# Kernel tuning notes

Hardware: AMD Instinct MI355X
Metric: run time of the kernel (lower is better)

Reference implementation:

```python
import jax, jax.numpy as jnp
import numpy as np

B, S, D, H, HD = 2, 2048, 1024, 16, 64


def setup_inputs() -> dict:
    key = jax.random.key(0)
    ks = jax.random.split(key, 11)
    scale_in = 1.0 / np.sqrt(D)
    return {
        "query": jax.random.normal(ks[0], (B, S, D), jnp.float32),
        "key": jax.random.normal(ks[1], (B, S, D), jnp.float32),
        "value": jax.random.normal(ks[2], (B, S, D), jnp.float32),
        "Wq": jax.random.normal(ks[3], (H, D, HD), jnp.float32) * scale_in,
        "bq": jax.random.normal(ks[4], (H, HD), jnp.float32) * 0.02,
        "Wk": jax.random.normal(ks[5], (H, D, HD), jnp.float32) * scale_in,
        "bk": jax.random.normal(ks[6], (H, HD), jnp.float32) * 0.02,
        "Wv": jax.random.normal(ks[7], (H, D, HD), jnp.float32) * scale_in,
        "bv": jax.random.normal(ks[8], (H, HD), jnp.float32) * 0.02,
        "Wo": jax.random.normal(ks[9], (D, D), jnp.float32) * scale_in,
        "bo": jax.random.normal(ks[10], (D,), jnp.float32) * 0.02,
    }


def reference(query, key, value, Wq, bq, Wk, bk, Wv, bv, Wo, bo):
    # Per-head projections, batched over heads (equivalent to the ModuleList loop).
    q = jnp.einsum('bsd,hdk->bhsk', query, Wq) + bq[None, :, None, :]   # [B,H,S,HD]
    k = jnp.einsum('bsd,hdk->bhsk', key, Wk) + bk[None, :, None, :]
    v = jnp.einsum('bsd,hdk->bhsk', value, Wv) + bv[None, :, None, :]
    scale = 1.0 / jnp.sqrt(jnp.asarray(q.shape[-1], q.dtype))
    scores = jnp.einsum('bhsk,bhtk->bhst', q, k) * scale                # [B,H,S,S]
    attn = jax.nn.softmax(scores, axis=-1)
    ctx = jnp.einsum('bhst,bhtk->bhsk', attn, v)                        # [B,H,S,HD]
    # Concat heads along last dim: [B,S,H*HD] == [B,S,D]
    x = jnp.transpose(ctx, (0, 2, 1, 3)).reshape(ctx.shape[0], ctx.shape[2], -1)
    return x @ Wo + bo
```

## Files before the change

kernel.cpp:

```cpp
#include <hip/hip_runtime.h>
#include <hip/hip_bf16.h>

typedef __bf16 bf16;
typedef __bf16 bf16x8 __attribute__((ext_vector_type(8)));
typedef __bf16 bf16x4 __attribute__((ext_vector_type(4)));
typedef __bf16 bf16x2 __attribute__((ext_vector_type(2)));
typedef float floatx4 __attribute__((ext_vector_type(4)));
typedef float floatx16 __attribute__((ext_vector_type(16)));

#define B_SZ 2
#define S_LEN 2048
#define D_DIM 1024
#define H_CNT 16
#define HD_DIM 64
#define M_ROWS 4096
#define QSCALE 0.18033688011112042f

__device__ __forceinline__ void async_ld16(const bf16* g, bf16* s) {
    __builtin_amdgcn_global_load_lds((const __attribute__((address_space(1))) void*)g,
                                     (__attribute__((address_space(3))) void*)s, 16, 0, 0);
}

__device__ __forceinline__ floatx4 mfma16(bf16x8 a, bf16x8 b, floatx4 c) {
    return __builtin_amdgcn_mfma_f32_16x16x32_bf16(a, b, c, 0, 0, 0);
}
__device__ __forceinline__ floatx16 mfma32(bf16x8 a, bf16x8 b, floatx16 c) {
    return __builtin_amdgcn_mfma_f32_32x32x16_bf16(a, b, c, 0, 0, 0);
}

struct PrepArgs {
    const float* cast_src[3]; bf16* cast_dst[3];
    const float* w_src[3];    bf16* w_dst[3];
    const float* wo;          bf16* wo_t;
};
__global__ __launch_bounds__(256) void prep(PrepArgs a) {
    __shared__ bf16 tile[32][33];
    const int bx = blockIdx.x, tid = threadIdx.x;
    if (bx < 12288) {
        const int t = bx >> 12, blk = bx & 4095;
        const float* s = a.cast_src[t];
        bf16* d = a.cast_dst[t];
        size_t i = ((size_t)blk * 256 + tid) * 4;
        float4 v = *(const float4*)(s + i);
        bf16x4 o = { (bf16)v.x, (bf16)v.y, (bf16)v.z, (bf16)v.w };
        *(bf16x4*)(d + i) = o;
        return;
    }
    int tx = tid & 31, ty = tid >> 5;
    const float* src; bf16* dst; int r0, c0, C, R;
    if (bx < 15360) {
        int idx = bx - 12288;
        int z = idx >> 6, xy = idx & 63;
        int mat = z >> 4, head = z & 15;
        src = a.w_src[mat] + (size_t)head * D_DIM * HD_DIM;
        dst = a.w_dst[mat] + (size_t)head * D_DIM * HD_DIM;
        r0 = (xy & 31) * 32; c0 = (xy >> 5) * 32; C = HD_DIM; R = D_DIM;
    } else {
        int idx = bx - 15360;
        src = a.wo; dst = a.wo_t;
        r0 = (idx & 31) * 32; c0 = (idx >> 5) * 32; C = D_DIM; R = D_DIM;
    }
#pragma unroll
    for (int i = 0; i < 32; i += 8)
        tile[ty + i][tx] = (bf16)src[(size_t)(r0 + ty + i) * C + c0 + tx];
    __syncthreads();
#pragma unroll
    for (int i = 0; i < 32; i += 8)
        dst[(size_t)(c0 + ty + i) * R + r0 + tx] = tile[tx][ty + i];
}

__global__ __launch_bounds__(256) void transpose2d(const bf16* __restrict__ src,
                                                   bf16* __restrict__ dst, int R, int C) {
    __shared__ bf16 tile[32][33];
    size_t zoff = (size_t)blockIdx.z * R * C;
    src += zoff; dst += zoff;
    int r0 = blockIdx.x * 32, c0 = blockIdx.y * 32;
    int tx = threadIdx.x & 31, ty = threadIdx.x >> 5;
#pragma unroll
    for (int i = 0; i < 32; i += 8) tile[ty + i][tx] = src[(size_t)(r0 + ty + i) * C + c0 + tx];
    __syncthreads();
#pragma unroll
    for (int i = 0; i < 32; i += 8) dst[(size_t)(c0 + ty + i) * R + r0 + tx] = tile[tx][ty + i];
}

struct GemmPtrs { const bf16* A; const bf16* BT; const float* bias; bf16* C; float* Cf; float scale; };
struct GemmArgs { GemmPtrs p[3]; int mode; };

__global__ __launch_bounds__(256) void gemm_bt(GemmArgs args) {
    __shared__ __align__(16) bf16 As[128 * 32];
    __shared__ __align__(16) bf16 Bs[128 * 32];
    const GemmPtrs P = args.p[blockIdx.z];
    const int tid = threadIdx.x, wave = tid >> 6, lane = tid & 63;
    const int quad = lane >> 4, l15 = lane & 15;
    const int bm = blockIdx.x * 128, bn = blockIdx.y * 128;
    const int wm = (wave >> 1) * 64, wn = (wave & 1) * 64;

    floatx4 acc[4][4];
#pragma unroll
    for (int i = 0; i < 4; i++)
#pragma unroll
        for (int j = 0; j < 4; j++) acc[i][j] = (floatx4){0.f, 0.f, 0.f, 0.f};

    const int srow = (lane >> 2);
    const int scol = (((lane & 3) ^ ((srow >> 1) & 3)) << 3);
    const int ck = ((quad ^ ((l15 >> 1) & 3)) << 3);
    for (int k0 = 0; k0 < 1024; k0 += 32) {
#pragma unroll
        for (int it = 0; it < 2; ++it) {
            int issue = it * 4 + wave;
            int row = issue * 16 + srow;
            async_ld16(P.A + (size_t)(bm + row) * 1024 + k0 + scol, &As[issue * 512]);
            async_ld16(P.BT + (size_t)(bn + row) * 1024 + k0 + scol, &Bs[issue * 512]);
        }
        __syncthreads();
        bf16x8 af[4], bfr[4];
#pragma unroll
        for (int mi = 0; mi < 4; mi++)
            af[mi] = *(const bf16x8*)&As[(wm + mi * 16 + l15) * 32 + ck];
#pragma unroll
        for (int ni = 0; ni < 4; ni++)
            bfr[ni] = *(const bf16x8*)&Bs[(wn + ni * 16 + l15) * 32 + ck];
#pragma unroll
        for (int mi = 0; mi < 4; mi++)
#pragma unroll
            for (int ni = 0; ni < 4; ni++) acc[mi][ni] = mfma16(af[mi], bfr[ni], acc[mi][ni]);
        __syncthreads();
    }
#pragma unroll
    for (int ni = 0; ni < 4; ni++) {
        int col = bn + wn + ni * 16 + l15;
        float bb = P.bias[col];
#pragma unroll
        for (int mi = 0; mi < 4; mi++) {
#pragma unroll
            for (int r = 0; r < 4; r++) {
                int row = bm + wm + mi * 16 + quad * 4 + r;
                float v = (acc[mi][ni][r] + bb) * P.scale;
                if (args.mode == 0) {
                    P.Cf[(size_t)row * 1024 + col] = v;
                } else {
                    int b = row >> 11, s2 = row & 2047, h = col >> 6, hd = col & 63;
                    P.C[(((size_t)(b * H_CNT + h)) * S_LEN + s2) * HD_DIM + hd] = (bf16)v;
                }
            }
        }
    }
}

__global__ __launch_bounds__(256) void attn(const bf16* __restrict__ Qg, const bf16* __restrict__ Kg,
                                            const bf16* __restrict__ Vtg, bf16* __restrict__ ctx) {
    __shared__ __align__(16) bf16 Ks[2][8192];
    __shared__ __align__(16) bf16 Vs[2][8192];
    __shared__ __align__(16) bf16 Ps[4][2048];
    const int tid = threadIdx.x, wave = tid >> 6, lane = tid & 63;
    const int l31 = lane & 31, half = lane >> 5;
    const int bid = blockIdx.x;
    const int bh = (bid >> 1) & 31;
    const int qb = ((bid >> 6) << 1) | (bid & 1);
    const int q0blk = qb * 128;
    const bf16* Kp = Kg + (size_t)bh * S_LEN * HD_DIM;
    const bf16* Vp = Vtg + (size_t)bh * HD_DIM * S_LEN;

#pragma unroll
    for (int it = 0; it < 4; ++it) {
        int i = it * 4 + wave;
        int f = i * 512 + lane * 8;
        int sub = f >> 12, rem = f & 4095;
        int c = rem >> 9, r = (rem >> 3) & 63;
        async_ld16(Kp + (size_t)(sub * 64 + r) * HD_DIM + c * 8, &Ks[0][i * 512]);
        async_ld16(Vp + (size_t)r * S_LEN + sub * 64 + c * 8, &Vs[0][i * 512]);
    }
    bf16x8 qf[4];
    {
        const bf16* qrow = Qg + ((size_t)bh * S_LEN + q0blk + wave * 32 + l31) * HD_DIM;
#pragma unroll
        for (int kb = 0; kb < 4; ++kb)
            qf[kb] = *(const bf16x8*)(qrow + (2 * kb + half) * 8);
    }
    __syncthreads();

    bf16* Pw = Ps[wave];
    float l_i = 0.f;
    floatx16 o0 = {0}, o1 = {0};

    for (int rd = 0; rd < 16; ++rd) {
        const int cur = rd & 1;
        if (rd < 15) {
            int t0n = (rd + 1) * 128;
#pragma unroll
            for (int it = 0; it < 4; ++it) {
                int i = it * 4 + wave;
                int f = i * 512 + lane * 8;
                int sub = f >> 12, rem = f & 4095;
                int c = rem >> 9, r = (rem >> 3) & 63;
                async_ld16(Kp + (size_t)(t0n + sub * 64 + r) * HD_DIM + c * 8, &Ks[cur ^ 1][i * 512]);
                async_ld16(Vp + (size_t)r * S_LEN + t0n + sub * 64 + c * 8, &Vs[cur ^ 1][i * 512]);
            }
        }
#pragma unroll
        for (int sub = 0; sub < 2; ++sub) {
            const bf16* Kt = &Ks[cur][sub * 4096];
            const bf16* Vt = &Vs[cur][sub * 4096];
            floatx16 sc0 = {0}, sc1 = {0};
#pragma unroll
            for (int kb = 0; kb < 4; ++kb) {
                bf16x8 k0 = *(const bf16x8*)&Kt[(2 * kb + half) * 512 + l31 * 8];
                bf16x8 k1 = *(const bf16x8*)&Kt[(2 * kb + half) * 512 + (32 + l31) * 8];
                sc0 = mfma32(k0, qf[kb], sc0);
                sc1 = mfma32(k1, qf[kb], sc1);
            }
            float rs = 0.f;
#pragma unroll
            for (int e = 0; e < 16; e += 2) {
                float p0 = __builtin_amdgcn_exp2f(sc0[e]);
                float p1 = __builtin_amdgcn_exp2f(sc0[e + 1]);
                rs += p0 + p1;
                *(bf16x2*)&Pw[(e >> 2) * 256 + l31 * 8 + (e & 3) + 4 * half] = (bf16x2){(bf16)p0, (bf16)p1};
            }
#pragma unroll
            for (int e = 0; e < 16; e += 2) {
                float p0 = __builtin_amdgcn_exp2f(sc1[e]);
                float p1 = __builtin_amdgcn_exp2f(sc1[e + 1]);
                rs += p0 + p1;
                *(bf16x2*)&Pw[(4 + (e >> 2)) * 256 + l31 * 8 + (e & 3) + 4 * half] = (bf16x2){(bf16)p0, (bf16)p1};
            }
            l_i += rs;
#pragma unroll
            for (int kb = 0; kb < 4; ++kb) {
                bf16x8 pf = *(const bf16x8*)&Pw[(2 * kb + half) * 256 + l31 * 8];
                bf16x8 v0 = *(const bf16x8*)&Vt[(2 * kb + half) * 512 + l31 * 8];
                bf16x8 v1 = *(const bf16x8*)&Vt[(2 * kb + half) * 512 + (32 + l31) * 8];
                o0 = mfma32(v0, pf, o0);
                o1 = mfma32(v1, pf, o1);
            }
        }
        __syncthreads();
    }
    l_i += __shfl_xor(l_i, 32);
    int b = bh >> 4, hh = bh & 15;
    float inv = 1.f / l_i;
#pragma unroll
    for (int s2 = 0; s2 < 2; ++s2) {
        const floatx16 oo = s2 ? o1 : o0;
#pragma unroll
        for (int e = 0; e < 16; ++e) {
            int hd = (e & 3) + 8 * (e >> 2) + 4 * half;
            Pw[l31 * 40 + hd] = (bf16)(oo[e] * inv);
        }
#pragma unroll
        for (int p = 0; p < 2; ++p) {
            int q = p * 16 + (lane >> 2), part = lane & 3;
            bf16x8 v = *(const bf16x8*)&Pw[q * 40 + part * 8];
            int s = q0blk + wave * 32 + q;
            *(bf16x8*)&ctx[((size_t)(b * S_LEN + s)) * D_DIM + hh * 64 + s2 * 32 + part * 8] = v;
        }
    }
}

extern "C" void kernel_launch(void* const* d_in, const int* in_sizes, int n_in,
                              void* d_out, int out_size, void* d_ws, size_t ws_size,
                              hipStream_t stream) {
    const float* query = (const float*)d_in[0];
    const float* key   = (const float*)d_in[1];
    const float* value = (const float*)d_in[2];
    const float* Wq = (const float*)d_in[3];
    const float* bq = (const float*)d_in[4];
    const float* Wk = (const float*)d_in[5];
    const float* bk = (const float*)d_in[6];
    const float* Wv = (const float*)d_in[7];
    const float* bv = (const float*)d_in[8];
    const float* Wo = (const float*)d_in[9];
    const float* bo = (const float*)d_in[10];
    float* out = (float*)d_out;

    bf16* ws = (bf16*)d_ws;
    const size_t ASZ = (size_t)M_ROWS * D_DIM;
    const size_t WSZ = (size_t)H_CNT * D_DIM * HD_DIM;
    const size_t TSZ = (size_t)B_SZ * H_CNT * S_LEN * HD_DIM;
    bf16* Qc  = ws;
    bf16* Kc  = Qc + ASZ;
    bf16* Vc  = Kc + ASZ;
    bf16* WqT = Vc + ASZ;
    bf16* WkT = WqT + WSZ;
    bf16* WvT = WkT + WSZ;
    bf16* WoT = WvT + WSZ;
    bf16* Qb  = WoT + (size_t)D_DIM * D_DIM;
    bf16* Kb  = Qb + TSZ;
    bf16* Vb  = Kb + TSZ;
    bf16* Vtb = Vb + TSZ;
    bf16* ctx = Vtb + TSZ;

    dim3 blk(256);

    PrepArgs pa;
    pa.cast_src[0] = query; pa.cast_src[1] = key; pa.cast_src[2] = value;
    pa.cast_dst[0] = Qc;    pa.cast_dst[1] = Kc;  pa.cast_dst[2] = Vc;
    pa.w_src[0] = Wq; pa.w_src[1] = Wk; pa.w_src[2] = Wv;
    pa.w_dst[0] = WqT; pa.w_dst[1] = WkT; pa.w_dst[2] = WvT;
    pa.wo = Wo; pa.wo_t = WoT;
    prep<<<dim3(16384), blk, 0, stream>>>(pa);

    GemmArgs qkv;
    qkv.p[0] = {Qc, WqT, bq, Qb, nullptr, QSCALE};
    qkv.p[1] = {Kc, WkT, bk, Kb, nullptr, 1.0f};
    qkv.p[2] = {Vc, WvT, bv, Vb, nullptr, 1.0f};
    qkv.mode = 1;
    gemm_bt<<<dim3(32, 8, 3), blk, 0, stream>>>(qkv);

    transpose2d<<<dim3(64, 2, 32), blk, 0, stream>>>(Vb, Vtb, 2048, 64);

    attn<<<dim3(512), blk, 0, stream>>>(Qb, Kb, Vtb, ctx);

    GemmArgs og;
    og.p[0] = {ctx, WoT, bo, nullptr, out, 1.0f};
    og.p[1] = og.p[0]; og.p[2] = og.p[0];
    og.mode = 0;
    gemm_bt<<<dim3(32, 8, 1), blk, 0, stream>>>(og);
}
```

Before: 244.4 us.

## Split attention key range across two blocks and double-buffer GEMM LDS tiles

The attention kernel now splits the key sequence into two halves, each handled by a separate block (1024 blocks instead of 512) with a smaller 64-key tile and less LDS per block. Each half writes unnormalized fp32 partial outputs and row sums to scratch, and a new combine kernel sums them, normalizes and writes bf16 context. This aims at higher occupancy and more parallel blocks, at the cost of extra global traffic and a launch. The GEMM also gains double-buffered LDS with prefetch of the next K tile to overlap loads with MFMA.

```diff
diff --git a/kernel.cpp b/kernel.cpp
--- a/kernel.cpp
+++ b/kernel.cpp
@@ -87,8 +87,8 @@
 struct GemmArgs { GemmPtrs p[3]; int mode; };
 
 __global__ __launch_bounds__(256) void gemm_bt(GemmArgs args) {
-    __shared__ __align__(16) bf16 As[128 * 32];
-    __shared__ __align__(16) bf16 Bs[128 * 32];
+    __shared__ __align__(16) bf16 As[2][4096];
+    __shared__ __align__(16) bf16 Bs[2][4096];
     const GemmPtrs P = args.p[blockIdx.z];
     const int tid = threadIdx.x, wave = tid >> 6, lane = tid & 63;
     const int quad = lane >> 4, l15 = lane & 15;
@@ -104,22 +104,35 @@
     const int srow = (lane >> 2);
     const int scol = (((lane & 3) ^ ((srow >> 1) & 3)) << 3);
     const int ck = ((quad ^ ((l15 >> 1) & 3)) << 3);
-    for (int k0 = 0; k0 < 1024; k0 += 32) {
-#pragma unroll
-        for (int it = 0; it < 2; ++it) {
-            int issue = it * 4 + wave;
-            int row = issue * 16 + srow;
-            async_ld16(P.A + (size_t)(bm + row) * 1024 + k0 + scol, &As[issue * 512]);
-            async_ld16(P.BT + (size_t)(bn + row) * 1024 + k0 + scol, &Bs[issue * 512]);
-        }
-        __syncthreads();
+
+#pragma unroll
+    for (int it = 0; it < 2; ++it) {
+        int issue = it * 4 + wave;
+        int row = issue * 16 + srow;
+        async_ld16(P.A + (size_t)(bm + row) * 1024 + scol, &As[0][issue * 512]);
+        async_ld16(P.BT + (size_t)(bn + row) * 1024 + scol, &Bs[0][issue * 512]);
+    }
+    __syncthreads();
+
+    for (int i = 0; i < 32; ++i) {
+        const int cur = i & 1;
+        if (i < 31) {
+            int k0 = (i + 1) * 32;
+#pragma unroll
+            for (int it = 0; it < 2; ++it) {
+                int issue = it * 4 + wave;
+                int row = issue * 16 + srow;
+                async_ld16(P.A + (size_t)(bm + row) * 1024 + k0 + scol, &As[cur ^ 1][issue * 512]);
+                async_ld16(P.BT + (size_t)(bn + row) * 1024 + k0 + scol, &Bs[cur ^ 1][issue * 512]);
+            }
+        }
         bf16x8 af[4], bfr[4];
 #pragma unroll
         for (int mi = 0; mi < 4; mi++)
-            af[mi] = *(const bf16x8*)&As[(wm + mi * 16 + l15) * 32 + ck];
+            af[mi] = *(const bf16x8*)&As[cur][(wm + mi * 16 + l15) * 32 + ck];
 #pragma unroll
         for (int ni = 0; ni < 4; ni++)
-            bfr[ni] = *(const bf16x8*)&Bs[(wn + ni * 16 + l15) * 32 + ck];
+            bfr[ni] = *(const bf16x8*)&Bs[cur][(wn + ni * 16 + l15) * 32 + ck];
 #pragma unroll
         for (int mi = 0; mi < 4; mi++)
 #pragma unroll
@@ -148,27 +161,30 @@
 }
 
 __global__ __launch_bounds__(256) void attn(const bf16* __restrict__ Qg, const bf16* __restrict__ Kg,
-                                            const bf16* __restrict__ Vtg, bf16* __restrict__ ctx) {
-    __shared__ __align__(16) bf16 Ks[2][8192];
-    __shared__ __align__(16) bf16 Vs[2][8192];
-    __shared__ __align__(16) bf16 Ps[4][2048];
+                                            const bf16* __restrict__ Vtg,
+                                            float* __restrict__ Op, float* __restrict__ lp) {
+    __shared__ __align__(16) bf16 SMEM[24576];
+    bf16* KsP = SMEM;
+    bf16* VsP = SMEM + 8192;
+    bf16* PsP = SMEM + 16384;
     const int tid = threadIdx.x, wave = tid >> 6, lane = tid & 63;
     const int l31 = lane & 31, half = lane >> 5;
     const int bid = blockIdx.x;
     const int bh = (bid >> 1) & 31;
-    const int qb = ((bid >> 6) << 1) | (bid & 1);
+    const int tp = bid & 1;
+    const int qb = bid >> 6;
     const int q0blk = qb * 128;
+    const int tbase0 = tp * 1024;
     const bf16* Kp = Kg + (size_t)bh * S_LEN * HD_DIM;
     const bf16* Vp = Vtg + (size_t)bh * HD_DIM * S_LEN;
 
 #pragma unroll
-    for (int it = 0; it < 4; ++it) {
+    for (int it = 0; it < 2; ++it) {
         int i = it * 4 + wave;
         int f = i * 512 + lane * 8;
-        int sub = f >> 12, rem = f & 4095;
-        int c = rem >> 9, r = (rem >> 3) & 63;
-        async_ld16(Kp + (size_t)(sub * 64 + r) * HD_DIM + c * 8, &Ks[0][i * 512]);
-        async_ld16(Vp + (size_t)r * S_LEN + sub * 64 + c * 8, &Vs[0][i * 512]);
+        int c = f >> 9, r = (f & 511) >> 3;
+        async_ld16(Kp + (size_t)(tbase0 + r) * HD_DIM + c * 8, &KsP[i * 512]);
+        async_ld16(Vp + (size_t)r * S_LEN + tbase0 + c * 8, &VsP[i * 512]);
     }
     bf16x8 qf[4];
     {
@@ -179,82 +195,96 @@
     }
     __syncthreads();
 
-    bf16* Pw = Ps[wave];
+    bf16* Pw = PsP + wave * 2048;
     float l_i = 0.f;
     floatx16 o0 = {0}, o1 = {0};
 
     for (int rd = 0; rd < 16; ++rd) {
         const int cur = rd & 1;
         if (rd < 15) {
-            int t0n = (rd + 1) * 128;
-#pragma unroll
-            for (int it = 0; it < 4; ++it) {
+            int t0n = tbase0 + (rd + 1) * 64;
+#pragma unroll
+            for (int it = 0; it < 2; ++it) {
                 int i = it * 4 + wave;
                 int f = i * 512 + lane * 8;
-                int sub = f >> 12, rem = f & 4095;
-                int c = rem >> 9, r = (rem >> 3) & 63;
-                async_ld16(Kp + (size_t)(t0n + sub * 64 + r) * HD_DIM + c * 8, &Ks[cur ^ 1][i * 512]);
-                async_ld16(Vp + (size_t)r * S_LEN + t0n + sub * 64 + c * 8, &Vs[cur ^ 1][i * 512]);
+                int c = f >> 9, r = (f & 511) >> 3;
+                async_ld16(Kp + (size_t)(t0n + r) * HD_DIM + c * 8, &KsP[(cur ^ 1) * 4096 + i * 512]);
+                async_ld16(Vp + (size_t)r * S_LEN + t0n + c * 8, &VsP[(cur ^ 1) * 4096 + i * 512]);
             }
         }
-#pragma unroll
-        for (int sub = 0; sub < 2; ++sub) {
-            const bf16* Kt = &Ks[cur][sub * 4096];
-            const bf16* Vt = &Vs[cur][sub * 4096];
-            floatx16 sc0 = {0}, sc1 = {0};
-#pragma unroll
-            for (int kb = 0; kb < 4; ++kb) {
-                bf16x8 k0 = *(const bf16x8*)&Kt[(2 * kb + half) * 512 + l31 * 8];
-                bf16x8 k1 = *(const bf16x8*)&Kt[(2 * kb + half) * 512 + (32 + l31) * 8];
-                sc0 = mfma32(k0, qf[kb], sc0);
-                sc1 = mfma32(k1, qf[kb], sc1);
-            }
-            float rs = 0.f;
-#pragma unroll
-            for (int e = 0; e < 16; e += 2) {
-                float p0 = __builtin_amdgcn_exp2f(sc0[e]);
-                float p1 = __builtin_amdgcn_exp2f(sc0[e + 1]);
-                rs += p0 + p1;
-                *(bf16x2*)&Pw[(e >> 2) * 256 + l31 * 8 + (e & 3) + 4 * half] = (bf16x2){(bf16)p0, (bf16)p1};
-            }
-#pragma unroll
-            for (int e = 0; e < 16; e += 2) {
-                float p0 = __builtin_amdgcn_exp2f(sc1[e]);
-                float p1 = __builtin_amdgcn_exp2f(sc1[e + 1]);
-                rs += p0 + p1;
-                *(bf16x2*)&Pw[(4 + (e >> 2)) * 256 + l31 * 8 + (e & 3) + 4 * half] = (bf16x2){(bf16)p0, (bf16)p1};
-            }
-            l_i += rs;
-#pragma unroll
-            for (int kb = 0; kb < 4; ++kb) {
-                bf16x8 pf = *(const bf16x8*)&Pw[(2 * kb + half) * 256 + l31 * 8];
-                bf16x8 v0 = *(const bf16x8*)&Vt[(2 * kb + half) * 512 + l31 * 8];
-                bf16x8 v1 = *(const bf16x8*)&Vt[(2 * kb + half) * 512 + (32 + l31) * 8];
-                o0 = mfma32(v0, pf, o0);
-                o1 = mfma32(v1, pf, o1);
-            }
+        const bf16* Kt = &KsP[cur * 4096];
+        const bf16* Vt = &VsP[cur * 4096];
+        floatx16 sc0 = {0}, sc1 = {0};
+#pragma unroll
+        for (int kb = 0; kb < 4; ++kb) {
+            bf16x8 k0 = *(const bf16x8*)&Kt[(2 * kb + half) * 512 + l31 * 8];
+            bf16x8 k1 = *(const bf16x8*)&Kt[(2 * kb + half) * 512 + (32 + l31) * 8];
+            sc0 = mfma32(k0, qf[kb], sc0);
+            sc1 = mfma32(k1, qf[kb], sc1);
+        }
+        float rs = 0.f;
+#pragma unroll
+        for (int e = 0; e < 16; e += 2) {
+            float p0 = __builtin_amdgcn_exp2f(sc0[e]);
+            float p1 = __builtin_amdgcn_exp2f(sc0[e + 1]);
+            rs += p0 + p1;
+            *(bf16x2*)&Pw[(e >> 2) * 256 + l31 * 8 + (e & 3) + 4 * half] = (bf16x2){(bf16)p0, (bf16)p1};
+        }
+#pragma unroll
+        for (int e = 0; e < 16; e += 2) {
+            float p0 = __builtin_amdgcn_exp2f(sc1[e]);
+            float p1 = __builtin_amdgcn_exp2f(sc1[e + 1]);
+            rs += p0 + p1;
+            *(bf16x2*)&Pw[(4 + (e >> 2)) * 256 + l31 * 8 + (e & 3) + 4 * half] = (bf16x2){(bf16)p0, (bf16)p1};
+        }
+        l_i += rs;
+#pragma unroll
+        for (int kb = 0; kb < 4; ++kb) {
+            bf16x8 pf = *(const bf16x8*)&Pw[(2 * kb + half) * 256 + l31 * 8];
+            bf16x8 v0 = *(const bf16x8*)&Vt[(2 * kb + half) * 512 + l31 * 8];
+            bf16x8 v1 = *(const bf16x8*)&Vt[(2 * kb + half) * 512 + (32 + l31) * 8];
+            o0 = mfma32(v0, pf, o0);
+            o1 = mfma32(v1, pf, o1);
         }
         __syncthreads();
     }
     l_i += __shfl_xor(l_i, 32);
-    int b = bh >> 4, hh = bh & 15;
-    float inv = 1.f / l_i;
+    float* slab = (float*)SMEM + wave * 1184;
+    const int s_base = q0blk + wave * 32;
 #pragma unroll
     for (int s2 = 0; s2 < 2; ++s2) {
         const floatx16 oo = s2 ? o1 : o0;
 #pragma unroll
         for (int e = 0; e < 16; ++e) {
             int hd = (e & 3) + 8 * (e >> 2) + 4 * half;
-            Pw[l31 * 40 + hd] = (bf16)(oo[e] * inv);
+            slab[l31 * 36 + hd] = oo[e];
         }
 #pragma unroll
         for (int p = 0; p < 2; ++p) {
             int q = p * 16 + (lane >> 2), part = lane & 3;
-            bf16x8 v = *(const bf16x8*)&Pw[q * 40 + part * 8];
-            int s = q0blk + wave * 32 + q;
-            *(bf16x8*)&ctx[((size_t)(b * S_LEN + s)) * D_DIM + hh * 64 + s2 * 32 + part * 8] = v;
-        }
-    }
+            float4 va = *(const float4*)&slab[q * 36 + part * 8];
+            float4 vb = *(const float4*)&slab[q * 36 + part * 8 + 4];
+            float* dst = Op + ((size_t)(tp * 32 + bh) * S_LEN + s_base + q) * HD_DIM + s2 * 32 + part * 8;
+            *(float4*)dst = va;
+            *(float4*)(dst + 4) = vb;
+        }
+    }
+    if (half == 0) lp[tp * 65536 + bh * S_LEN + s_base + l31] = l_i;
+}
+
+__global__ __launch_bounds__(256) void combine(const float* __restrict__ Op,
+                                               const float* __restrict__ lp,
+                                               bf16* __restrict__ ctx) {
+    int idx = blockIdx.x * 256 + threadIdx.x;
+    int sg = idx >> 4;
+    int hd = (idx & 15) * 4;
+    float4 a = *(const float4*)&Op[(size_t)sg * 64 + hd];
+    float4 b = *(const float4*)&Op[4194304 + (size_t)sg * 64 + hd];
+    float inv = 1.f / (lp[sg] + lp[65536 + sg]);
+    int bb = sg >> 15, h = (sg >> 11) & 15, sl = sg & 2047;
+    bf16x4 o = { (bf16)((a.x + b.x) * inv), (bf16)((a.y + b.y) * inv),
+                 (bf16)((a.z + b.z) * inv), (bf16)((a.w + b.w) * inv) };
+    *(bf16x4*)&ctx[((size_t)(bb * S_LEN + sl)) * D_DIM + h * HD_DIM + hd] = o;
 }
 
 extern "C" void kernel_launch(void* const* d_in, const int* in_sizes, int n_in,
@@ -273,22 +303,23 @@
     const float* bo = (const float*)d_in[10];
     float* out = (float*)d_out;
 
-    bf16* ws = (bf16*)d_ws;
-    const size_t ASZ = (size_t)M_ROWS * D_DIM;
-    const size_t WSZ = (size_t)H_CNT * D_DIM * HD_DIM;
-    const size_t TSZ = (size_t)B_SZ * H_CNT * S_LEN * HD_DIM;
-    bf16* Qc  = ws;
-    bf16* Kc  = Qc + ASZ;
-    bf16* Vc  = Kc + ASZ;
-    bf16* WqT = Vc + ASZ;
-    bf16* WkT = WqT + WSZ;
-    bf16* WvT = WkT + WSZ;
-    bf16* WoT = WvT + WSZ;
-    bf16* Qb  = WoT + (size_t)D_DIM * D_DIM;
-    bf16* Kb  = Qb + TSZ;
-    bf16* Vb  = Kb + TSZ;
-    bf16* Vtb = Vb + TSZ;
-    bf16* ctx = Vtb + TSZ;
+    bf16* ws0 = (bf16*)d_ws;
+    const size_t M1 = 1u << 20;
+    bf16* WoT = ws0;
+    bf16* Qb  = WoT + M1;
+    bf16* Kb  = Qb + 4 * M1;
+    bf16* Vtb = Kb + 4 * M1;
+    bf16* SCR = Vtb + 4 * M1;
+    bf16* Qc  = SCR;
+    bf16* Kc  = Qc + 4 * M1;
+    bf16* Vc  = Kc + 4 * M1;
+    bf16* WqT = Vc + 4 * M1;
+    bf16* WkT = WqT + M1;
+    bf16* WvT = WkT + M1;
+    bf16* Vb  = WvT + M1;
+    bf16* ctx = Vb + 4 * M1;
+    float* Op = (float*)SCR;
+    float* lp = Op + 8388608;
 
     dim3 blk(256);
 
@@ -309,7 +340,9 @@
 
     transpose2d<<<dim3(64, 2, 32), blk, 0, stream>>>(Vb, Vtb, 2048, 64);
 
-    attn<<<dim3(512), blk, 0, stream>>>(Qb, Kb, Vtb, ctx);
+    attn<<<dim3(1024), blk, 0, stream>>>(Qb, Kb, Vtb, Op, lp);
+
+    combine<<<dim3(4096), blk, 0, stream>>>(Op, lp, ctx);
 
     GemmArgs og;
     og.p[0] = {ctx, WoT, bo, nullptr, out, 1.0f};
```

Result: slower. 250.8 us (+2.6%).
